# Kernel optimization log

Hardware: AMD Instinct MI355X
Metric: run time of the kernel (lower is better)

## Reference

```python
import jax, jax.numpy as jnp
import numpy as np
from jax import lax

K = 3      # kernel size
PAD = 1    # padding (stride=1, dilation=1, single offset group)


def _deform_conv2d(x, off, weight, bias):
    # x: [B,C,H,W], off: [B,2*K*K,H,W] (y,x per tap), weight: [O,C,K,K], bias: [O]
    B, C, H, W = x.shape
    KK = K * K
    off = off.reshape(B, KK, 2, H, W)
    off_y, off_x = off[:, :, 0], off[:, :, 1]          # [B,KK,H,W]

    kh = jnp.repeat(jnp.arange(K, dtype=x.dtype), K)   # [KK] tap row offsets
    kw = jnp.tile(jnp.arange(K, dtype=x.dtype), K)     # [KK] tap col offsets
    py = (jnp.arange(H, dtype=x.dtype)[None, None, :, None] - PAD
          + kh[None, :, None, None] + off_y)           # [B,KK,H,W] sample rows
    px = (jnp.arange(W, dtype=x.dtype)[None, None, None, :] - PAD
          + kw[None, :, None, None] + off_x)           # [B,KK,H,W] sample cols

    y0 = jnp.floor(py); x0 = jnp.floor(px)
    wy1 = py - y0; wx1 = px - x0
    wy0 = 1.0 - wy1; wx0 = 1.0 - wx1

    bidx = jnp.arange(B)[:, None, None, None]

    def gather(iy, ix):
        # zero outside the input (torchvision semantics)
        valid = (iy >= 0) & (iy < H) & (ix >= 0) & (ix < W)
        iyc = jnp.clip(iy, 0, H - 1).astype(jnp.int32)
        ixc = jnp.clip(ix, 0, W - 1).astype(jnp.int32)
        v = x[bidx, :, iyc, ixc]                       # [B,KK,H,W,C]
        return v * valid[..., None].astype(x.dtype)

    samp = (gather(y0, x0)           * (wy0 * wx0)[..., None]
            + gather(y0, x0 + 1)     * (wy0 * wx1)[..., None]
            + gather(y0 + 1, x0)     * (wy1 * wx0)[..., None]
            + gather(y0 + 1, x0 + 1) * (wy1 * wx1)[..., None])  # [B,KK,H,W,C]

    w = weight.reshape(weight.shape[0], C, KK)          # [O,C,KK]
    out = jnp.einsum('bkhwc,ock->bohw', samp, w) + bias[None, :, None, None]
    return out


def setup_inputs() -> dict:
    key = jax.random.key(0)
    k1, k2, k3 = jax.random.split(key, 3)
    B, C, O, H, W = 4, 64, 64, 128, 128
    x = jax.random.normal(k1, (B, C, H, W), dtype=jnp.float32)
    offset_w = jax.random.normal(k2, (2 * K * K, C, 3, 3), dtype=jnp.float32) * 0.02
    offset_b = jnp.zeros((2 * K * K,), dtype=jnp.float32)
    weight = jax.random.normal(k3, (O, C, K, K), dtype=jnp.float32) * 0.01
    bias = jnp.zeros((O,), dtype=jnp.float32)
    return {"x": x, "offset_w": offset_w, "offset_b": offset_b,
            "weight": weight, "bias": bias}


def reference(x, offset_w, offset_b, weight, bias):
    # offset-predicting conv (3x3, pad 1)
    off = lax.conv_general_dilated(
        x, offset_w, window_strides=(1, 1), padding='SAME',
        dimension_numbers=('NCHW', 'OIHW', 'NCHW')) + offset_b[None, :, None, None]
    return _deform_conv2d(x, off, weight, bias)
```

## Files before the change

### kernel.cpp

```cpp
#include <hip/hip_runtime.h>
#include <hip/hip_bf16.h>


typedef short short8 __attribute__((ext_vector_type(8)));
typedef short short4v __attribute__((ext_vector_type(4)));
typedef float f32x4 __attribute__((ext_vector_type(4)));

static __device__ inline short bf16s(float f) {
    __hip_bfloat16 h = __float2bfloat16(f);
    return *(short*)&h;
}
static __device__ inline float lo2f(unsigned u) { return __uint_as_float(u << 16); }
static __device__ inline float hi2f(unsigned u) { return __uint_as_float(u & 0xffff0000u); }

__global__ void prep_transpose_kernel(const float* __restrict__ x,
                                      __hip_bfloat16* __restrict__ xBp,
                                      const float* __restrict__ offset_w,
                                      const float* __restrict__ weight,
                                      __hip_bfloat16* __restrict__ Wb,
                                      __hip_bfloat16* __restrict__ OWb)
{
    __shared__ __align__(16) float lds[128 * 65];
    int raw = blockIdx.x;
    int t = threadIdx.x;

    if (raw >= 520) {
        int id = (raw - 520) * 256 + t;
        if (id < 36864) {
            int j    = id & 7;
            int lane = (id >> 3) & 63;
            int id3  = id >> 9;
            int s    = id3 % 18;
            int otile = id3 / 18;
            int n = lane & 15, q = lane >> 4;
            int kap = s * 32 + q * 8 + j;
            int k = kap >> 6, c = kap & 63;
            int o = otile * 16 + n;
            Wb[id] = __float2bfloat16(weight[(o * 64 + c) * 9 + k]);
        }
        int id2 = id - 36864;
        if (id2 >= 0 && id2 < 18432) {
            int j    = id2 & 7;
            int lane = (id2 >> 3) & 63;
            int id3  = id2 >> 9;
            int s    = id3 % 18;
            int ntile = id3 / 18;
            int n = lane & 15, q = lane >> 4;
            int kap = s * 32 + q * 8 + j;
            int k = kap >> 6, c = kap & 63;
            int o = ntile * 16 + n;
            float v = (o < 18) ? offset_w[(o * 64 + c) * 9 + k] : 0.0f;
            OWb[id2] = __float2bfloat16(v);
        }
        return;
    }

    int blk = (raw & 7) * 65 + (raw >> 3);
    int b = blk / 130, r = blk - b * 130;
    unsigned* rowp = (unsigned*)(xBp + (size_t)(b * 130 + r) * 130 * 64);
    if (r == 0 || r == 129) {
        uint4 z = {0u, 0u, 0u, 0u};
        for (int i = 0; i < 5; ++i) {
            int e = i * 256 + t;
            if (e < 1040) ((uint4*)rowp)[e] = z;
        }
        return;
    }
    int h = r - 1;
    int w = t & 127, chalf = t >> 7;
    for (int i = 0; i < 32; ++i) {
        int c = i * 2 + chalf;
        lds[w * 65 + c] = x[((b * 64 + c) * 128 + h) * 128 + w];
    }
    __syncthreads();
    unsigned* dst = rowp + 32;
    for (int i = 0; i < 16; ++i) {
        int L = i * 256 + t;
        int ww = L >> 5, c2 = L & 31;
        float f0 = lds[ww * 65 + c2 * 2];
        float f1 = lds[ww * 65 + c2 * 2 + 1];
        unsigned pk = ((unsigned)bf16s(f0) & 0xffffu) | ((unsigned)bf16s(f1) << 16);
        dst[L] = pk;
    }
    if (t < 64) {
        int col = (t >> 5) * 129;
        rowp[col * 32 + (t & 31)] = 0u;
    }
}

__global__ __launch_bounds__(256, 4) void offconv_kernel(
    const __hip_bfloat16* __restrict__ xBp,
    const __hip_bfloat16* __restrict__ OWb,
    const float* __restrict__ offset_b,
    float* __restrict__ off_g)
{
    __shared__ __align__(16) short patch[198 * 80];

    int t = threadIdx.x, wv = t >> 6, lane = t & 63;
    int bid = (blockIdx.x & 7) * 128 + (blockIdx.x >> 3);
    int half = bid & 1;
    int bh = bid >> 1;
    int b = bh >> 7, h = bh & 127;
    int w0 = half * 64;

    for (int i = 0; i < 7; ++i) {
        int e = i * 256 + t;
        if (e < 1584) {
            int px = e >> 3, part = e & 7;
            int prow = px / 66, pcol = px - prow * 66;
            const uint4* src = (const uint4*)(xBp +
                (size_t)((b * 130 + h + prow) * 130 + w0 + pcol) * 64 + part * 8);
            *(uint4*)&patch[px * 80 + part * 8] = *src;
        }
    }
    __syncthreads();

    int n = lane & 15, q = lane >> 4;
    const short8* Bw = (const short8*)OWb;
    f32x4 acc0 = {0.f, 0.f, 0.f, 0.f};
    f32x4 acc1 = {0.f, 0.f, 0.f, 0.f};
#pragma unroll
    for (int s = 0; s < 18; ++s) {
        int k = s >> 1;
        int ky = k / 3, kx = k - ky * 3;
        int pix = ky * 66 + wv * 16 + n + kx;
        const short8 a = *(const short8*)&patch[pix * 80 + (s & 1) * 32 + q * 8];
        acc0 = __builtin_amdgcn_mfma_f32_16x16x32_bf16(a, Bw[(0 * 18 + s) * 64 + lane], acc0, 0, 0, 0);
        acc1 = __builtin_amdgcn_mfma_f32_16x16x32_bf16(a, Bw[(1 * 18 + s) * 64 + lane], acc1, 0, 0, 0);
    }
    float* og = off_g + ((size_t)(b * 128 + h) * 18) * 128 + w0 + wv * 16 + q * 4;
    {
        float bo = offset_b[n];
        float4 st = {acc0[0] + bo, acc0[1] + bo, acc0[2] + bo, acc0[3] + bo};
        *(float4*)&og[n * 128] = st;
    }
    if (n < 2) {
        int o = 16 + n;
        float bo = offset_b[o];
        float4 st = {acc1[0] + bo, acc1[1] + bo, acc1[2] + bo, acc1[3] + bo};
        *(float4*)&og[o * 128] = st;
    }
}

__global__ __launch_bounds__(256, 6) void deform_kernel(
    const __hip_bfloat16* __restrict__ xBp,
    const __hip_bfloat16* __restrict__ Wb,
    const float* __restrict__ off_g,
    const float* __restrict__ bias,
    float* __restrict__ out)
{
    __shared__ __align__(16) short sampB[18 * 16 * 40];
    __shared__ __align__(16) float offL[288];

    int t = threadIdx.x, wv = t >> 6, lane = t & 63;
    int bid = (blockIdx.x & 7) * 512 + (blockIdx.x >> 3);
    int b  = bid >> 10;
    int h  = (bid >> 3) & 127;
    int w0 = (bid & 7) << 4;

    for (int e = t; e < 288; e += 256) {
        int o = e >> 4, p = e & 15;
        offL[o * 16 + p] = off_g[((size_t)((b * 128 + h) * 18 + o)) * 128 + w0 + p];
    }
    __syncthreads();

    {
        int g = lane >> 4, c4 = lane & 15;
        int p = wv * 4 + g;
        const __hip_bfloat16* xb4 = xBp + (size_t)b * (130 * 130 * 64) + c4 * 4 + 131 * 64;

        float offy[9], offx[9];
#pragma unroll
        for (int k = 0; k < 9; ++k) {
            offy[k] = offL[(2 * k) * 16 + p];
            offx[k] = offL[(2 * k + 1) * 16 + p];
        }

#pragma unroll
        for (int k = 0; k < 9; ++k) {
            float py = (float)(h - 1 + (k / 3)) + offy[k];
            float px = (float)(w0 + p - 1 + (k % 3)) + offx[k];
            float y0f = floorf(py), x0f = floorf(px);
            float wy1 = py - y0f, wx1 = px - x0f;
            float wy0 = 1.0f - wy1, wx0 = 1.0f - wx1;
            int iy = (int)y0f, ix = (int)x0f;
            int iy0 = min(max(iy, -1), 128);
            int ix0 = min(max(ix, -1), 128);
            int iy1 = min(max(iy + 1, -1), 128);
            int ix1 = min(max(ix + 1, -1), 128);
            int rb0 = iy0 * 130, rb1 = iy1 * 130;
            int e00 = (rb0 + ix0) * 64;
            int e01 = (rb0 + ix1) * 64;
            int e10 = (rb1 + ix0) * 64;
            int e11 = (rb1 + ix1) * 64;
            float wa  = wy0 * wx0;
            float wb_ = wy0 * wx1;
            float wc  = wy1 * wx0;
            float wd  = wy1 * wx1;

            uint2 r0 = *(const uint2*)(xb4 + e00);
            uint2 r1 = *(const uint2*)(xb4 + e01);
            uint2 r2 = *(const uint2*)(xb4 + e10);
            uint2 r3 = *(const uint2*)(xb4 + e11);

            float s0 = fmaf(wd, lo2f(r3.x), fmaf(wc, lo2f(r2.x), fmaf(wb_, lo2f(r1.x), wa * lo2f(r0.x))));
            float s1 = fmaf(wd, hi2f(r3.x), fmaf(wc, hi2f(r2.x), fmaf(wb_, hi2f(r1.x), wa * hi2f(r0.x))));
            float s2 = fmaf(wd, lo2f(r3.y), fmaf(wc, lo2f(r2.y), fmaf(wb_, lo2f(r1.y), wa * lo2f(r0.y))));
            float s3 = fmaf(wd, hi2f(r3.y), fmaf(wc, hi2f(r2.y), fmaf(wb_, hi2f(r1.y), wa * hi2f(r0.y))));
            int s = 2 * k + (c4 >> 3);
            short4v pk = { bf16s(s0), bf16s(s1), bf16s(s2), bf16s(s3) };
            *(short4v*)&sampB[(s * 16 + p) * 40 + (c4 & 7) * 4] = pk;
        }
    }
    __syncthreads();

    {
        int n = lane & 15, q = lane >> 4;
        int arow = n * 40 + q * 8;
        const short8* BwW = (const short8*)Wb + (wv * 18) * 64 + lane;
        f32x4 acc = {0.f, 0.f, 0.f, 0.f};
#pragma unroll
        for (int s = 0; s < 18; ++s) {
            const short8 a = *(const short8*)&sampB[s * 640 + arow];
            acc = __builtin_amdgcn_mfma_f32_16x16x32_bf16(a, BwW[s * 64], acc, 0, 0, 0);
        }
        int o = wv * 16 + n;
        float bo = bias[o];
        float4 st = {acc[0] + bo, acc[1] + bo, acc[2] + bo, acc[3] + bo};
        *(float4*)&out[(((size_t)b * 64 + o) * 128 + h) * 128 + w0 + q * 4] = st;
    }
}

extern "C" void kernel_launch(void* const* d_in, const int* in_sizes, int n_in,
                              void* d_out, int out_size, void* d_ws, size_t ws_size,
                              hipStream_t stream) {
    const float* x        = (const float*)d_in[0];
    const float* offset_w = (const float*)d_in[1];
    const float* offset_b = (const float*)d_in[2];
    const float* weight   = (const float*)d_in[3];
    const float* bias     = (const float*)d_in[4];
    char* ws = (char*)d_ws;
    __hip_bfloat16* xBp = (__hip_bfloat16*)ws;
    __hip_bfloat16* Wb  = (__hip_bfloat16*)(ws + 8652800);
    __hip_bfloat16* OWb = (__hip_bfloat16*)(ws + 8652800 + 73728);
    float* off_g        = (float*)(ws + 8652800 + 73728 + 36864);
    float* outp = (float*)d_out;

    hipLaunchKernelGGL(prep_transpose_kernel, dim3(736),  dim3(256), 0, stream,
                       x, xBp, offset_w, weight, Wb, OWb);
    hipLaunchKernelGGL(offconv_kernel,        dim3(1024), dim3(256), 0, stream, xBp, OWb, offset_b, off_g);
    hipLaunchKernelGGL(deform_kernel,         dim3(4096), dim3(256), 0, stream, xBp, Wb, off_g, bias, outp);
}
```

Before: 117.5 us.

## Fuse offset-predicting conv into deform kernel, dropping separate launch and offset buffer

The offset convolution kernel is removed. Each deform block now loads a 3x18 pixel halo patch of the bf16 padded input into shared memory (reusing the sampling buffer) and computes its own 18 offsets for 16 pixels with MFMA on two waves. This removes one kernel launch and the global write and read of the offset tensor. In exchange, halo loads are repeated across neighbouring blocks, two of four waves idle during the offset phase, and an extra barrier is added.

```diff
diff --git a/kernel.cpp b/kernel.cpp
--- a/kernel.cpp
+++ b/kernel.cpp
@@ -88,64 +88,11 @@
     }
 }
 
-__global__ __launch_bounds__(256, 4) void offconv_kernel(
-    const __hip_bfloat16* __restrict__ xBp,
-    const __hip_bfloat16* __restrict__ OWb,
-    const float* __restrict__ offset_b,
-    float* __restrict__ off_g)
-{
-    __shared__ __align__(16) short patch[198 * 80];
-
-    int t = threadIdx.x, wv = t >> 6, lane = t & 63;
-    int bid = (blockIdx.x & 7) * 128 + (blockIdx.x >> 3);
-    int half = bid & 1;
-    int bh = bid >> 1;
-    int b = bh >> 7, h = bh & 127;
-    int w0 = half * 64;
-
-    for (int i = 0; i < 7; ++i) {
-        int e = i * 256 + t;
-        if (e < 1584) {
-            int px = e >> 3, part = e & 7;
-            int prow = px / 66, pcol = px - prow * 66;
-            const uint4* src = (const uint4*)(xBp +
-                (size_t)((b * 130 + h + prow) * 130 + w0 + pcol) * 64 + part * 8);
-            *(uint4*)&patch[px * 80 + part * 8] = *src;
-        }
-    }
-    __syncthreads();
-
-    int n = lane & 15, q = lane >> 4;
-    const short8* Bw = (const short8*)OWb;
-    f32x4 acc0 = {0.f, 0.f, 0.f, 0.f};
-    f32x4 acc1 = {0.f, 0.f, 0.f, 0.f};
-#pragma unroll
-    for (int s = 0; s < 18; ++s) {
-        int k = s >> 1;
-        int ky = k / 3, kx = k - ky * 3;
-        int pix = ky * 66 + wv * 16 + n + kx;
-        const short8 a = *(const short8*)&patch[pix * 80 + (s & 1) * 32 + q * 8];
-        acc0 = __builtin_amdgcn_mfma_f32_16x16x32_bf16(a, Bw[(0 * 18 + s) * 64 + lane], acc0, 0, 0, 0);
-        acc1 = __builtin_amdgcn_mfma_f32_16x16x32_bf16(a, Bw[(1 * 18 + s) * 64 + lane], acc1, 0, 0, 0);
-    }
-    float* og = off_g + ((size_t)(b * 128 + h) * 18) * 128 + w0 + wv * 16 + q * 4;
-    {
-        float bo = offset_b[n];
-        float4 st = {acc0[0] + bo, acc0[1] + bo, acc0[2] + bo, acc0[3] + bo};
-        *(float4*)&og[n * 128] = st;
-    }
-    if (n < 2) {
-        int o = 16 + n;
-        float bo = offset_b[o];
-        float4 st = {acc1[0] + bo, acc1[1] + bo, acc1[2] + bo, acc1[3] + bo};
-        *(float4*)&og[o * 128] = st;
-    }
-}
-
 __global__ __launch_bounds__(256, 6) void deform_kernel(
     const __hip_bfloat16* __restrict__ xBp,
     const __hip_bfloat16* __restrict__ Wb,
-    const float* __restrict__ off_g,
+    const __hip_bfloat16* __restrict__ OWb,
+    const float* __restrict__ offset_b,
     const float* __restrict__ bias,
     float* __restrict__ out)
 {
@@ -158,9 +105,42 @@
     int h  = (bid >> 3) & 127;
     int w0 = (bid & 7) << 4;
 
-    for (int e = t; e < 288; e += 256) {
-        int o = e >> 4, p = e & 15;
-        offL[o * 16 + p] = off_g[((size_t)((b * 128 + h) * 18 + o)) * 128 + w0 + p];
+    short* patch = sampB;
+
+    {
+#pragma unroll
+        for (int i = 0; i < 2; ++i) {
+            int e = i * 256 + t;
+            if (e < 432) {
+                int px = e >> 3, part = e & 7;
+                int row = px / 18, col = px - row * 18;
+                const uint4* src = (const uint4*)(xBp +
+                    ((size_t)((b * 130 + h + row) * 130) + w0 + col) * 64 + part * 8);
+                *(uint4*)&patch[px * 80 + part * 8] = *src;
+            }
+        }
+    }
+    __syncthreads();
+
+    if (wv < 2) {
+        int n = lane & 15, q = lane >> 4;
+        const short8* Bw = (const short8*)OWb + (wv * 18) * 64 + lane;
+        f32x4 acc = {0.f, 0.f, 0.f, 0.f};
+#pragma unroll
+        for (int s = 0; s < 18; ++s) {
+            int k = s >> 1;
+            int ky = k / 3, kx = k - ky * 3;
+            int pix = ky * 18 + n + kx;
+            const short8 a = *(const short8*)&patch[pix * 80 + (s & 1) * 32 + q * 8];
+            acc = __builtin_amdgcn_mfma_f32_16x16x32_bf16(a, Bw[s * 64], acc, 0, 0, 0);
+        }
+        int o = wv * 16 + n;
+        if (o < 18) {
+            float bo = offset_b[o];
+#pragma unroll
+            for (int r = 0; r < 4; ++r)
+                offL[o * 16 + q * 4 + r] = acc[r] + bo;
+        }
     }
     __syncthreads();
 
@@ -243,11 +223,10 @@
     __hip_bfloat16* xBp = (__hip_bfloat16*)ws;
     __hip_bfloat16* Wb  = (__hip_bfloat16*)(ws + 8652800);
     __hip_bfloat16* OWb = (__hip_bfloat16*)(ws + 8652800 + 73728);
-    float* off_g        = (float*)(ws + 8652800 + 73728 + 36864);
     float* outp = (float*)d_out;
 
     hipLaunchKernelGGL(prep_transpose_kernel, dim3(736),  dim3(256), 0, stream,
                        x, xBp, offset_w, weight, Wb, OWb);
-    hipLaunchKernelGGL(offconv_kernel,        dim3(1024), dim3(256), 0, stream, xBp, OWb, offset_b, off_g);
-    hipLaunchKernelGGL(deform_kernel,         dim3(4096), dim3(256), 0, stream, xBp, Wb, off_g, bias, outp);
-}
+    hipLaunchKernelGGL(deform_kernel,         dim3(4096), dim3(256), 0, stream,
+                       xBp, Wb, OWb, offset_b, bias, outp);
+}
```

Measured after the change: 111.8 us. 4.8% less time.
